# Performance work log

Measured on AMD Instinct MI355X. Metric: run time of the kernel, lower is better.

## Reference

```python
import jax, jax.numpy as jnp
import numpy as np

H = 4  # pairwise_num_attention_heads

def _layer_norm(x, gamma, beta, eps=1e-5):
    mu = jnp.mean(x, axis=-1, keepdims=True)
    var = jnp.var(x, axis=-1, keepdims=True)
    return (x - mu) * jax.lax.rsqrt(var + eps) * gamma + beta

def setup_inputs() -> dict:
    key = jax.random.key(0)
    ks = jax.random.split(key, 8)
    B, L, P = 1, 256, 128
    s = 0.02
    return {
        "pairwise_states": jax.random.normal(ks[0], (B, L, L, P), jnp.float32),
        "ln_gamma": jnp.ones((P,), jnp.float32),
        "ln_beta": jnp.zeros((P,), jnp.float32),
        "Wq": jax.random.normal(ks[1], (P, P), jnp.float32) * s,
        "Wk": jax.random.normal(ks[2], (P, P), jnp.float32) * s,
        "Wv": jax.random.normal(ks[3], (P, P), jnp.float32) * s,
        "Wb": jax.random.normal(ks[4], (P, H), jnp.float32) * s,
        "Wg": jax.random.normal(ks[5], (P, P), jnp.float32) * s,
        "bg": jnp.zeros((P,), jnp.float32),
        "Wo": jax.random.normal(ks[6], (P, P), jnp.float32) * s,
        "bo": jnp.zeros((P,), jnp.float32),
    }

def reference(pairwise_states, ln_gamma, ln_beta, Wq, Wk, Wv, Wb, Wg, bg, Wo, bo):
    # Row-axis triangle attention (RibonanzaNetPairwiseAttention, axis='row', eval mode).
    B, L, _, P = pairwise_states.shape
    D = P // H  # attention_head_size
    x = _layer_norm(pairwise_states, ln_gamma, ln_beta)  # [b,i,j,p]
    q = (x @ Wq).reshape(B, L, L, H, D)
    k = (x @ Wk).reshape(B, L, L, H, D)
    v = (x @ Wv).reshape(B, L, L, H, D)
    scale = jnp.asarray(D, x.dtype) ** 0.5
    # pairwise bias: [b,i,j,h] -> broadcast over the row axis of the scores
    bias = jnp.einsum('bijp,ph->bhij', x, Wb)  # [b,h,L,L]
    # scores[b,h,i,j,k]: within row i, query position j attends to key position k
    scores = jnp.einsum('bijhd,bikhd->bhijk', q, k) / scale + bias[:, :, None]
    probs = jax.nn.softmax(scores, axis=-1)
    ctx = jnp.einsum('bhijk,bikhd->bijhd', probs, v).reshape(B, L, L, P)
    gate = jax.nn.sigmoid(x @ Wg + bg)
    ctx = gate * ctx
    # output dense + residual (AxisDropout is identity in eval mode)
    return ctx @ Wo + bo + pairwise_states
```

## Files before the change

kernel.cpp:

```cpp
#include <hip/hip_runtime.h>

#define NPOS 65536

typedef __attribute__((ext_vector_type(8))) short bf16x8;
typedef __attribute__((ext_vector_type(4))) float f32x4;

#if __has_builtin(__builtin_amdgcn_exp2f)
#define EXP2F(x) __builtin_amdgcn_exp2f(x)
#else
#define EXP2F(x) __expf((x) * 0.6931471805599453f)
#endif
#if __has_builtin(__builtin_amdgcn_rcpf)
#define RCPF(x) __builtin_amdgcn_rcpf(x)
#else
#define RCPF(x) (1.0f / (x))
#endif

static __device__ __forceinline__ unsigned short f2bf(float f) {
  union { float f; unsigned int u; } v; v.f = f;
  unsigned int r = v.u + 0x7fffu + ((v.u >> 16) & 1u);
  return (unsigned short)(r >> 16);
}
static __device__ __forceinline__ unsigned int pack2(float a, float b) {
  return (unsigned int)f2bf(a) | ((unsigned int)f2bf(b) << 16);
}
static __device__ __forceinline__ float lo_bf(unsigned int u) {
  union { unsigned int u; float f; } v; v.u = u << 16; return v.f;
}
static __device__ __forceinline__ float hi_bf(unsigned int u) {
  union { unsigned int u; float f; } v; v.u = u & 0xffff0000u; return v.f;
}
static __device__ __forceinline__ unsigned int permpack(float hi, float lo) {
  union { float f; unsigned int u; } a, b;
  a.f = hi; b.f = lo;
#if __has_builtin(__builtin_amdgcn_perm)
  return __builtin_amdgcn_perm(a.u, b.u, 0x07060302u);
#else
  return (a.u & 0xffff0000u) | (b.u >> 16);
#endif
}

__global__ void k_pack(const float* __restrict__ Wq, const float* __restrict__ Wk,
                       const float* __restrict__ Wv, const float* __restrict__ Wg,
                       const float* __restrict__ Wo,
                       ushort* __restrict__ WT, ushort* __restrict__ WoT) {
  int idx = blockIdx.x * blockDim.x + threadIdx.x;
  if (idx < 512 * 128) {
    int n = idx >> 7, k = idx & 127;
    int nn = n & 127;
    float val;
    if (n < 128)      val = Wq[k * 128 + nn] * (0.17677669529663687f * 1.4426950408889634f);
    else if (n < 256) val = Wk[k * 128 + nn];
    else if (n < 384) val = Wv[k * 128 + nn];
    else              val = Wg[k * 128 + nn];
    WT[idx] = f2bf(val);
  } else if (idx < 512 * 128 + 128 * 128) {
    int j = idx - 512 * 128;
    int n = j >> 7, k = j & 127;
    WoT[j] = f2bf(Wo[k * 128 + n]);
  }
}

__global__ __launch_bounds__(128, 4) void k_ln(
    const float* __restrict__ in, const float* __restrict__ gamma,
    const float* __restrict__ beta, const float* __restrict__ Wb,
    ushort* __restrict__ xln, ushort* __restrict__ biasB) {
  int t = threadIdx.x, wv = t >> 6, lane = t & 63;
  int n = lane & 15, g = lane >> 4;
  int myrow = blockIdx.x * 32 + wv * 16 + n;
  const float* rp = in + (size_t)myrow * 128;

  float xv[32];
  float sm = 0.f, ssm = 0.f;
  #pragma unroll
  for (int kc = 0; kc < 4; kc++)
    #pragma unroll
    for (int pr = 0; pr < 2; pr++) {
      float4 v = *(const float4*)(rp + kc * 32 + g * 8 + pr * 4);
      int o = kc * 8 + pr * 4;
      xv[o] = v.x; xv[o+1] = v.y; xv[o+2] = v.z; xv[o+3] = v.w;
      sm  += v.x + v.y + v.z + v.w;
      ssm += v.x*v.x + v.y*v.y + v.z*v.z + v.w*v.w;
    }
  sm  += __shfl_xor(sm, 16, 64);  sm  += __shfl_xor(sm, 32, 64);
  ssm += __shfl_xor(ssm, 16, 64); ssm += __shfl_xor(ssm, 32, 64);
  float mu  = sm * (1.0f / 128.0f);
  float var = ssm * (1.0f / 128.0f) - mu * mu;
  float rs  = rsqrtf(var + 1e-5f);
  float p0 = 0.f, p1 = 0.f, p2 = 0.f, p3 = 0.f;
  #pragma unroll
  for (int kc = 0; kc < 4; kc++)
    #pragma unroll
    for (int pr = 0; pr < 2; pr++) {
      int c0 = kc * 32 + g * 8 + pr * 4;
      float4 g4 = *(const float4*)(gamma + c0);
      float4 b4 = *(const float4*)(beta + c0);
      int o = kc * 8 + pr * 4;
      #pragma unroll
      for (int r = 0; r < 4; r++) {
        float xn = (xv[o + r] - mu) * rs * (&g4.x)[r] + (&b4.x)[r];
        xv[o + r] = xn;
        float4 w = ((const float4*)Wb)[c0 + r];
        p0 += xn * w.x; p1 += xn * w.y; p2 += xn * w.z; p3 += xn * w.w;
      }
    }
  #pragma unroll
  for (int kc = 0; kc < 4; kc++)
    #pragma unroll
    for (int pr = 0; pr < 2; pr++) {
      int o = kc * 8 + pr * 4;
      uint2 px;
      px.x = pack2(xv[o + 1], xv[o]);
      px.x = (unsigned int)f2bf(xv[o]) | ((unsigned int)f2bf(xv[o + 1]) << 16);
      px.y = (unsigned int)f2bf(xv[o + 2]) | ((unsigned int)f2bf(xv[o + 3]) << 16);
      *(uint2*)(xln + (size_t)myrow * 128 + kc * 32 + g * 8 + pr * 4) = px;
    }
  p0 += __shfl_xor(p0, 16, 64); p0 += __shfl_xor(p0, 32, 64);
  p1 += __shfl_xor(p1, 16, 64); p1 += __shfl_xor(p1, 32, 64);
  p2 += __shfl_xor(p2, 16, 64); p2 += __shfl_xor(p2, 32, 64);
  p3 += __shfl_xor(p3, 16, 64); p3 += __shfl_xor(p3, 32, 64);
  if (g == 0) {
    const float l2e = 1.4426950408889634f;
    biasB[0 * NPOS + myrow] = f2bf(p0 * l2e);
    biasB[1 * NPOS + myrow] = f2bf(p1 * l2e);
    biasB[2 * NPOS + myrow] = f2bf(p2 * l2e);
    biasB[3 * NPOS + myrow] = f2bf(p3 * l2e);
  }
}

#define KS 40
#define VS 264
#define QS 40
#define PST 40
__global__ __launch_bounds__(512, 2) void k_attn2(
    const ushort* __restrict__ xln, const ushort* __restrict__ WT,
    const float* __restrict__ bg, const ushort* __restrict__ biasB,
    ushort* __restrict__ gctx) {
  __shared__ __align__(16) ushort Klds[256 * KS];
  __shared__ __align__(16) ushort VTlds[32 * VS];
  __shared__ __align__(16) ushort qstg[8][32 * QS];
  __shared__ __align__(16) ushort pstg[8][16 * PST];
  int i = blockIdx.x & 255, h = blockIdx.x >> 8;
  int t = threadIdx.x, wv = t >> 6, lane = t & 63;
  int n = lane & 15, g = lane >> 4;
  int r0 = wv * 32;

  bf16x8 a[2][4];
  const ushort* xb = xln + ((size_t)i * 256 + r0) * 128;
  #pragma unroll
  for (int c = 0; c < 2; c++)
    #pragma unroll
    for (int kc = 0; kc < 4; kc++)
      a[c][kc] = *(const bf16x8*)(xb + (size_t)(c * 16 + n) * 128 + kc * 32 + g * 8);

  f32x4 gs[2][2];
  #pragma unroll
  for (int sect = 0; sect < 4; sect++) {
    bf16x8 b[2][4];
    #pragma unroll
    for (int ntl = 0; ntl < 2; ntl++)
      #pragma unroll
      for (int kc = 0; kc < 4; kc++)
        b[ntl][kc] = *(const bf16x8*)(WT + (size_t)(sect * 128 + h * 32 + ntl * 16 + n) * 128 + kc * 32 + g * 8);
    #pragma unroll
    for (int c = 0; c < 2; c++) {
      f32x4 acc[2];
      #pragma unroll
      for (int ntl = 0; ntl < 2; ntl++) {
        f32x4 cc = {0.f, 0.f, 0.f, 0.f};
        #pragma unroll
        for (int kc = 0; kc < 4; kc++)
          cc = __builtin_amdgcn_mfma_f32_16x16x32_bf16(a[c][kc], b[ntl][kc], cc, 0, 0, 0);
        acc[ntl] = cc;
      }
      if (sect == 0) {
        #pragma unroll
        for (int ntl = 0; ntl < 2; ntl++)
          #pragma unroll
          for (int r = 0; r < 4; r++)
            qstg[wv][(c * 16 + g * 4 + r) * QS + ntl * 16 + n] = f2bf(acc[ntl][r]);
      } else if (sect == 1) {
        #pragma unroll
        for (int ntl = 0; ntl < 2; ntl++)
          #pragma unroll
          for (int r = 0; r < 4; r++)
            Klds[(r0 + c * 16 + g * 4 + r) * KS + ntl * 16 + n] = f2bf(acc[ntl][r]);
      } else if (sect == 2) {
        #pragma unroll
        for (int ntl = 0; ntl < 2; ntl++) {
          uint2 vp;
          vp.x = (unsigned int)f2bf(acc[ntl][0]) | ((unsigned int)f2bf(acc[ntl][1]) << 16);
          vp.y = (unsigned int)f2bf(acc[ntl][2]) | ((unsigned int)f2bf(acc[ntl][3]) << 16);
          *(uint2*)(&VTlds[(ntl * 16 + n) * VS + r0 + c * 16 + g * 4]) = vp;
        }
      } else {
        #pragma unroll
        for (int ntl = 0; ntl < 2; ntl++)
          #pragma unroll
          for (int r = 0; r < 4; r++)
            gs[c][ntl][r] = 1.0f / (1.0f + __expf(-(acc[ntl][r] + bg[h * 32 + ntl * 16 + n])));
      }
    }
  }
  __syncthreads();

  const ushort* bb = biasB + (size_t)h * NPOS;
  ushort* Pw = pstg[wv];
  #pragma unroll
  for (int tt = 0; tt < 2; tt++) {
    int j0 = r0 + tt * 16;
    bf16x8 bq = *(const bf16x8*)(&qstg[wv][(tt * 16 + n) * QS + g * 8]);
    uint2 bv[16];
    #pragma unroll
    for (int kt = 0; kt < 16; kt++)
      bv[kt] = *(const uint2*)(bb + (size_t)(j0 + n) * 256 + kt * 16 + g * 4);
    f32x4 s[16];
    #pragma unroll
    for (int kt = 0; kt < 16; kt++) {
      bf16x8 ak = *(const bf16x8*)(&Klds[(kt * 16 + n) * KS + g * 8]);
      f32x4 cc;
      cc[0] = lo_bf(bv[kt].x); cc[1] = hi_bf(bv[kt].x);
      cc[2] = lo_bf(bv[kt].y); cc[3] = hi_bf(bv[kt].y);
      s[kt] = __builtin_amdgcn_mfma_f32_16x16x32_bf16(ak, bq, cc, 0, 0, 0);
    }
    f32x4 a4 = {0.f, 0.f, 0.f, 0.f};
    #pragma unroll
    for (int kt = 0; kt < 16; kt++) {
      #pragma unroll
      for (int r = 0; r < 4; r++) s[kt][r] = EXP2F(s[kt][r]);
      a4 += s[kt];
    }
    float smm = (a4[0] + a4[1]) + (a4[2] + a4[3]);
    smm += __shfl_xor(smm, 16, 64);
    smm += __shfl_xor(smm, 32, 64);
    float inv = RCPF(smm);
    f32x4 ctx0 = {0.f, 0.f, 0.f, 0.f}, ctx1 = {0.f, 0.f, 0.f, 0.f};
    #pragma unroll
    for (int c8 = 0; c8 < 8; c8++) {
      #pragma unroll
      for (int t2 = 0; t2 < 2; t2++) {
        int kt = c8 * 2 + t2;
        uint2 pp;
        pp.x = permpack(s[kt][1] * inv, s[kt][0] * inv);
        pp.y = permpack(s[kt][3] * inv, s[kt][2] * inv);
        *(uint2*)(&Pw[n * PST + t2 * 16 + g * 4]) = pp;
      }
      bf16x8 ap = *(const bf16x8*)(&Pw[n * PST + g * 8]);
      bf16x8 v0 = *(const bf16x8*)(&VTlds[(size_t)n * VS + c8 * 32 + g * 8]);
      bf16x8 v1 = *(const bf16x8*)(&VTlds[(size_t)(16 + n) * VS + c8 * 32 + g * 8]);
      ctx0 = __builtin_amdgcn_mfma_f32_16x16x32_bf16(ap, v0, ctx0, 0, 0, 0);
      ctx1 = __builtin_amdgcn_mfma_f32_16x16x32_bf16(ap, v1, ctx1, 0, 0, 0);
    }
    #pragma unroll
    for (int r = 0; r < 4; r++) {
      size_t pos = (size_t)i * 256 + j0 + g * 4 + r;
      gctx[pos * 128 + h * 32 + n]      = f2bf(ctx0[r] * gs[tt][0][r]);
      gctx[pos * 128 + h * 32 + 16 + n] = f2bf(ctx1[r] * gs[tt][1][r]);
    }
  }
}

__global__ __launch_bounds__(128, 4) void k_out(
    const ushort* __restrict__ gctx, const ushort* __restrict__ WoT,
    const float* __restrict__ bo, const float* __restrict__ in0,
    float* __restrict__ out) {
  __shared__ __align__(16) float CT[16 * 132];
  int t = threadIdx.x, wv = t >> 6, lane = t & 63;
  int n = lane & 15, g = lane >> 4;
  int row0 = blockIdx.x * 16;
  bf16x8 a[4];
  #pragma unroll
  for (int kc = 0; kc < 4; kc++)
    a[kc] = *(const bf16x8*)(gctx + (size_t)(row0 + n) * 128 + kc * 32 + g * 8);
  #pragma unroll
  for (int ntl2 = 0; ntl2 < 4; ntl2++) {
    int ntl = wv * 4 + ntl2;
    f32x4 acc = {0.f, 0.f, 0.f, 0.f};
    #pragma unroll
    for (int kc = 0; kc < 4; kc++) {
      bf16x8 b = *(const bf16x8*)(WoT + (size_t)(ntl * 16 + n) * 128 + kc * 32 + g * 8);
      acc = __builtin_amdgcn_mfma_f32_16x16x32_bf16(a[kc], b, acc, 0, 0, 0);
    }
    float bov = bo[ntl * 16 + n];
    #pragma unroll
    for (int r = 0; r < 4; r++)
      CT[(g * 4 + r) * 132 + ntl * 16 + n] = acc[r] + bov;
  }
  __syncthreads();
  #pragma unroll
  for (int it = 0; it < 4; it++) {
    int c = it * 128 + t;
    int row = c >> 5, off = (c & 31) * 4;
    f32x4 v = *(const f32x4*)(&CT[row * 132 + off]);
    size_t o = (size_t)(row0 + row) * 128 + off;
    f32x4 r4 = *(const f32x4*)(in0 + o);
    v[0] += r4[0]; v[1] += r4[1]; v[2] += r4[2]; v[3] += r4[3];
    *(f32x4*)(out + o) = v;
  }
}

extern "C" void kernel_launch(void* const* d_in, const int* in_sizes, int n_in,
                              void* d_out, int out_size, void* d_ws, size_t ws_size,
                              hipStream_t stream) {
  const float* in0   = (const float*)d_in[0];
  const float* gamma = (const float*)d_in[1];
  const float* beta  = (const float*)d_in[2];
  const float* Wq    = (const float*)d_in[3];
  const float* Wk    = (const float*)d_in[4];
  const float* Wv    = (const float*)d_in[5];
  const float* Wb    = (const float*)d_in[6];
  const float* Wg    = (const float*)d_in[7];
  const float* bg    = (const float*)d_in[8];
  const float* Wo    = (const float*)d_in[9];
  const float* bo    = (const float*)d_in[10];
  float* out = (float*)d_out;
  char* ws = (char*)d_ws;

  const size_t MB = 1024 * 1024;
  ushort* gctx  = (ushort*)(ws);
  ushort* xln   = (ushort*)(ws + 16 * MB);
  ushort* biasB = (ushort*)(ws + 32 * MB);
  ushort* WT    = (ushort*)(ws + 33 * MB);
  ushort* WoT   = (ushort*)(ws + 33 * MB + 128 * 1024);

  k_pack <<<320, 256, 0, stream>>>(Wq, Wk, Wv, Wg, Wo, WT, WoT);
  k_ln   <<<2048, 128, 0, stream>>>(in0, gamma, beta, Wb, xln, biasB);
  k_attn2<<<1024, 512, 0, stream>>>(xln, WT, bg, biasB, gctx);
  k_out  <<<4096, 128, 0, stream>>>(gctx, WoT, bo, in0, out);
}
```

Measured before the change: 208.7 us.

## Keep softmax probs in registers for PV MFMA and drop LDS staging in output GEMM

In the attention kernel, the probability fragment for the PV MFMA is now packed directly from the score accumulators in registers instead of going through a per-wave LDS staging buffer. The V operand loads are split into two 8-byte reads so their k-ordering matches the register layout of the probabilities. The output projection kernel swaps the MFMA operand order so each lane holds 4 consecutive output columns, then adds bias and the residual and writes float4 directly, removing the shared-memory transpose and block barrier. It also uses 4 waves per block, each handling 16 rows. The cost is narrower LDS reads for V and a different global access pattern in the output kernel.

```diff
diff --git a/kernel.cpp b/kernel.cpp
--- a/kernel.cpp
+++ b/kernel.cpp
@@ -20,9 +20,6 @@
   union { float f; unsigned int u; } v; v.f = f;
   unsigned int r = v.u + 0x7fffu + ((v.u >> 16) & 1u);
   return (unsigned short)(r >> 16);
-}
-static __device__ __forceinline__ unsigned int pack2(float a, float b) {
-  return (unsigned int)f2bf(a) | ((unsigned int)f2bf(b) << 16);
 }
 static __device__ __forceinline__ float lo_bf(unsigned int u) {
   union { unsigned int u; float f; } v; v.u = u << 16; return v.f;
@@ -110,7 +107,6 @@
     for (int pr = 0; pr < 2; pr++) {
       int o = kc * 8 + pr * 4;
       uint2 px;
-      px.x = pack2(xv[o + 1], xv[o]);
       px.x = (unsigned int)f2bf(xv[o]) | ((unsigned int)f2bf(xv[o + 1]) << 16);
       px.y = (unsigned int)f2bf(xv[o + 2]) | ((unsigned int)f2bf(xv[o + 3]) << 16);
       *(uint2*)(xln + (size_t)myrow * 128 + kc * 32 + g * 8 + pr * 4) = px;
@@ -131,7 +127,6 @@
 #define KS 40
 #define VS 264
 #define QS 40
-#define PST 40
 __global__ __launch_bounds__(512, 2) void k_attn2(
     const ushort* __restrict__ xln, const ushort* __restrict__ WT,
     const float* __restrict__ bg, const ushort* __restrict__ biasB,
@@ -139,7 +134,6 @@
   __shared__ __align__(16) ushort Klds[256 * KS];
   __shared__ __align__(16) ushort VTlds[32 * VS];
   __shared__ __align__(16) ushort qstg[8][32 * QS];
-  __shared__ __align__(16) ushort pstg[8][16 * PST];
   int i = blockIdx.x & 255, h = blockIdx.x >> 8;
   int t = threadIdx.x, wv = t >> 6, lane = t & 63;
   int n = lane & 15, g = lane >> 4;
@@ -205,7 +199,6 @@
   __syncthreads();
 
   const ushort* bb = biasB + (size_t)h * NPOS;
-  ushort* Pw = pstg[wv];
   #pragma unroll
   for (int tt = 0; tt < 2; tt++) {
     int j0 = r0 + tt * 16;
@@ -237,19 +230,18 @@
     f32x4 ctx0 = {0.f, 0.f, 0.f, 0.f}, ctx1 = {0.f, 0.f, 0.f, 0.f};
     #pragma unroll
     for (int c8 = 0; c8 < 8; c8++) {
-      #pragma unroll
-      for (int t2 = 0; t2 < 2; t2++) {
-        int kt = c8 * 2 + t2;
-        uint2 pp;
-        pp.x = permpack(s[kt][1] * inv, s[kt][0] * inv);
-        pp.y = permpack(s[kt][3] * inv, s[kt][2] * inv);
-        *(uint2*)(&Pw[n * PST + t2 * 16 + g * 4]) = pp;
-      }
-      bf16x8 ap = *(const bf16x8*)(&Pw[n * PST + g * 8]);
-      bf16x8 v0 = *(const bf16x8*)(&VTlds[(size_t)n * VS + c8 * 32 + g * 8]);
-      bf16x8 v1 = *(const bf16x8*)(&VTlds[(size_t)(16 + n) * VS + c8 * 32 + g * 8]);
-      ctx0 = __builtin_amdgcn_mfma_f32_16x16x32_bf16(ap, v0, ctx0, 0, 0, 0);
-      ctx1 = __builtin_amdgcn_mfma_f32_16x16x32_bf16(ap, v1, ctx1, 0, 0, 0);
+      union { bf16x8 v; uint2 u[2]; } ap;
+      ap.u[0].x = permpack(s[c8*2][1] * inv, s[c8*2][0] * inv);
+      ap.u[0].y = permpack(s[c8*2][3] * inv, s[c8*2][2] * inv);
+      ap.u[1].x = permpack(s[c8*2+1][1] * inv, s[c8*2+1][0] * inv);
+      ap.u[1].y = permpack(s[c8*2+1][3] * inv, s[c8*2+1][2] * inv);
+      union { bf16x8 v; uint2 u[2]; } v0, v1;
+      v0.u[0] = *(const uint2*)(&VTlds[(size_t)n * VS + c8 * 32 + g * 4]);
+      v0.u[1] = *(const uint2*)(&VTlds[(size_t)n * VS + c8 * 32 + 16 + g * 4]);
+      v1.u[0] = *(const uint2*)(&VTlds[(size_t)(16 + n) * VS + c8 * 32 + g * 4]);
+      v1.u[1] = *(const uint2*)(&VTlds[(size_t)(16 + n) * VS + c8 * 32 + 16 + g * 4]);
+      ctx0 = __builtin_amdgcn_mfma_f32_16x16x32_bf16(ap.v, v0.v, ctx0, 0, 0, 0);
+      ctx1 = __builtin_amdgcn_mfma_f32_16x16x32_bf16(ap.v, v1.v, ctx1, 0, 0, 0);
     }
     #pragma unroll
     for (int r = 0; r < 4; r++) {
@@ -260,42 +252,32 @@
   }
 }
 
-__global__ __launch_bounds__(128, 4) void k_out(
+__global__ __launch_bounds__(256, 4) void k_out(
     const ushort* __restrict__ gctx, const ushort* __restrict__ WoT,
     const float* __restrict__ bo, const float* __restrict__ in0,
     float* __restrict__ out) {
-  __shared__ __align__(16) float CT[16 * 132];
   int t = threadIdx.x, wv = t >> 6, lane = t & 63;
   int n = lane & 15, g = lane >> 4;
-  int row0 = blockIdx.x * 16;
-  bf16x8 a[4];
+  int row0 = blockIdx.x * 64 + wv * 16;
+  bf16x8 cfr[4];
   #pragma unroll
   for (int kc = 0; kc < 4; kc++)
-    a[kc] = *(const bf16x8*)(gctx + (size_t)(row0 + n) * 128 + kc * 32 + g * 8);
-  #pragma unroll
-  for (int ntl2 = 0; ntl2 < 4; ntl2++) {
-    int ntl = wv * 4 + ntl2;
+    cfr[kc] = *(const bf16x8*)(gctx + (size_t)(row0 + n) * 128 + kc * 32 + g * 8);
+  size_t rowg = (size_t)row0 + n;
+  #pragma unroll
+  for (int ntl = 0; ntl < 8; ntl++) {
     f32x4 acc = {0.f, 0.f, 0.f, 0.f};
     #pragma unroll
     for (int kc = 0; kc < 4; kc++) {
-      bf16x8 b = *(const bf16x8*)(WoT + (size_t)(ntl * 16 + n) * 128 + kc * 32 + g * 8);
-      acc = __builtin_amdgcn_mfma_f32_16x16x32_bf16(a[kc], b, acc, 0, 0, 0);
-    }
-    float bov = bo[ntl * 16 + n];
-    #pragma unroll
-    for (int r = 0; r < 4; r++)
-      CT[(g * 4 + r) * 132 + ntl * 16 + n] = acc[r] + bov;
-  }
-  __syncthreads();
-  #pragma unroll
-  for (int it = 0; it < 4; it++) {
-    int c = it * 128 + t;
-    int row = c >> 5, off = (c & 31) * 4;
-    f32x4 v = *(const f32x4*)(&CT[row * 132 + off]);
-    size_t o = (size_t)(row0 + row) * 128 + off;
+      bf16x8 wo = *(const bf16x8*)(WoT + (size_t)(ntl * 16 + n) * 128 + kc * 32 + g * 8);
+      acc = __builtin_amdgcn_mfma_f32_16x16x32_bf16(wo, cfr[kc], acc, 0, 0, 0);
+    }
+    f32x4 b4 = *(const f32x4*)(bo + ntl * 16 + g * 4);
+    size_t o = rowg * 128 + ntl * 16 + g * 4;
     f32x4 r4 = *(const f32x4*)(in0 + o);
-    v[0] += r4[0]; v[1] += r4[1]; v[2] += r4[2]; v[3] += r4[3];
-    *(f32x4*)(out + o) = v;
+    acc[0] += b4[0] + r4[0]; acc[1] += b4[1] + r4[1];
+    acc[2] += b4[2] + r4[2]; acc[3] += b4[3] + r4[3];
+    *(f32x4*)(out + o) = acc;
   }
 }
 
@@ -326,5 +308,5 @@
   k_pack <<<320, 256, 0, stream>>>(Wq, Wk, Wv, Wg, Wo, WT, WoT);
   k_ln   <<<2048, 128, 0, stream>>>(in0, gamma, beta, Wb, xln, biasB);
   k_attn2<<<1024, 512, 0, stream>>>(xln, WT, bg, biasB, gctx);
-  k_out  <<<4096, 128, 0, stream>>>(gctx, WoT, bo, in0, out);
-}
+  k_out  <<<1024, 256, 0, stream>>>(gctx, WoT, bo, in0, out);
+}
```

After: 217.2 us. 1.04x slower.
